# Kernel optimization log

Measured on AMD Instinct MI355X. Metric: run time of the kernel, lower is better.

Reference implementation:

```python
import jax, jax.numpy as jnp
import numpy as np

EMBED = 1024
HEADS = 16
HEAD_DIM = EMBED // HEADS
BATCH = 2
SEQ = 256

def setup_inputs() -> dict:
    key = jax.random.key(0)
    ks = jax.random.split(key, 6)
    x = jax.random.normal(ks[0], (BATCH, SEQ, EMBED), dtype=jnp.float32)
    s = 1.0 / np.sqrt(HEAD_DIM)
    Wq = jax.random.uniform(ks[1], (HEAD_DIM, HEAD_DIM), jnp.float32, -s, s)
    Wk = jax.random.uniform(ks[2], (HEAD_DIM, HEAD_DIM), jnp.float32, -s, s)
    Wv = jax.random.uniform(ks[3], (HEAD_DIM, HEAD_DIM), jnp.float32, -s, s)
    so = 1.0 / np.sqrt(EMBED)
    Wo = jax.random.uniform(ks[4], (EMBED, EMBED), jnp.float32, -so, so)
    bo = jax.random.uniform(ks[5], (EMBED,), jnp.float32, -so, so)
    return {"x": x, "Wq": Wq, "Wk": Wk, "Wv": Wv, "Wo": Wo, "bo": bo}

def reference(x, Wq, Wk, Wv, Wo, bo):
    n, s, e = x.shape
    xr = x.reshape(n, s, HEADS, HEAD_DIM)          # (n,s,h,d)
    # nn.Linear applies x @ W.T
    q = jnp.einsum('nshd,ed->nshe', xr, Wq)
    k = jnp.einsum('nshd,ed->nshe', xr, Wk)
    v = jnp.einsum('nshd,ed->nshe', xr, Wv)
    # elementwise outer-product score: (n,s,t,h,d), no reduction over d
    energy = q[:, :, None, :, :] * k[:, None, :, :, :]
    # NOTE: original code softmaxes over dim=3 == the HEADS axis
    attn = jax.nn.softmax(energy / jnp.float32(np.sqrt(EMBED)), axis=3)
    out = jnp.einsum('nsthd,nthd->nshd', attn, v)  # reduce over t
    out = out.reshape(n, s, HEADS * HEAD_DIM)
    return out @ Wo.T + bo
```

## Files before the change

kernel.cpp:

```cpp
#include <hip/hip_runtime.h>

#define NB 2
#define SQL 256
#define NH 16
#define HD 64
#define EMB 1024

typedef unsigned short ushortT;
typedef unsigned int uintT;
typedef __attribute__((ext_vector_type(8))) short bf16x8;
typedef __attribute__((ext_vector_type(4))) float f32x4;
typedef __attribute__((ext_vector_type(2))) float f32x2;

__device__ __constant__ float kQSCALE = 1.4426950408889634f / 32.0f;

__device__ __forceinline__ float fexp2(float x) { return __builtin_amdgcn_exp2f(x); }
__device__ __forceinline__ float frcp(float x)  { return __builtin_amdgcn_rcpf(x); }

__device__ __forceinline__ ushortT f2bf(float x) {
    uintT u = __float_as_uint(x);
    u += 0x7fffu + ((u >> 16) & 1u);
    return (ushortT)(u >> 16);
}
__device__ __forceinline__ ushort4 f2bf4(float4 a) {
    return make_ushort4(f2bf(a.x), f2bf(a.y), f2bf(a.z), f2bf(a.w));
}
__device__ __forceinline__ f32x2 unpk2(uintT u) {
    f32x2 r;
    r.x = __uint_as_float(u << 16);
    r.y = __uint_as_float(u & 0xffff0000u);
    return r;
}
__device__ __forceinline__ float pairsum_dpp(float u) {
    const int j = __builtin_amdgcn_mov_dpp(__float_as_int(u), 0xB1, 0xF, 0xF, true);
    return u + __int_as_float(j);
}

__global__ __launch_bounds__(256) void qkv_kernel(
    const float* __restrict__ x,
    const float* __restrict__ Wq,
    const float* __restrict__ Wk,
    const float* __restrict__ Wv,
    const float* __restrict__ Wo,
    const float* __restrict__ bo,
    ushortT* __restrict__ Q,
    ushortT* __restrict__ K,
    ushortT* __restrict__ V,
    float* __restrict__ AO,
    float* __restrict__ out,
    ushortT* __restrict__ Wob)
{
    __shared__ ushortT wls[3][64 * 72];
    __shared__ ushortT xs[2][16 * 72];

    const int tid = threadIdx.x;
    const int ns0 = blockIdx.x * 2;
    const int g   = blockIdx.x * 256 + tid;

    {
        const float4 z = make_float4(0.f, 0.f, 0.f, 0.f);
        ((float4*)AO)[g] = z;
        ((float4*)AO)[g + 65536] = z;
        const float4 bb = ((const float4*)bo)[g & 255];
        ((float4*)out)[g] = bb;
        ((float4*)out)[g + 65536] = bb;
    }
#pragma unroll
    for (int j = 0; j < 4; ++j) {
        const int f4 = j * 65536 + g;
        ((ushort4*)Wob)[f4] = f2bf4(((const float4*)Wo)[f4]);
    }

#pragma unroll
    for (int m = 0; m < 3; ++m) {
        const float4* src = (m == 0) ? (const float4*)Wq
                          : (m == 1) ? (const float4*)Wk : (const float4*)Wv;
#pragma unroll
        for (int j = 0; j < 4; ++j) {
            const int idx = j * 256 + tid;
            const int e   = idx >> 4;
            const int d4  = idx & 15;
            float4 a = src[idx];
            if (m == 0) { a.x *= kQSCALE; a.y *= kQSCALE; a.z *= kQSCALE; a.w *= kQSCALE; }
            *(ushort4*)&wls[m][e * 72 + d4 * 4] = f2bf4(a);
        }
    }
#pragma unroll
    for (int j = 0; j < 2; ++j) {
        const int idx = j * 256 + tid;
        const int r   = idx >> 8;
        const int h   = (idx >> 4) & 15;
        const int d4  = idx & 15;
        const float4 a = ((const float4*)(x + (size_t)(ns0 + r) * EMB))[idx & 255];
        *(ushort4*)&xs[r][h * 72 + d4 * 4] = f2bf4(a);
    }
    __syncthreads();

    const int w   = tid >> 6;
    const int nsr = w >> 1;
    const int eb0 = (w & 1) * 32;
    const int l   = tid & 63;
    const int lr  = l & 15;
    const int lk  = l >> 4;

    const bf16x8 a0 = *(const bf16x8*)&xs[nsr][lr * 72 + lk * 8];
    const bf16x8 a1 = *(const bf16x8*)&xs[nsr][lr * 72 + 32 + lk * 8];

#pragma unroll
    for (int m = 0; m < 3; ++m) {
        ushortT* outp = (m == 0) ? Q : (m == 1) ? K : V;
#pragma unroll
        for (int ef = 0; ef < 2; ++ef) {
            const int eb = eb0 + ef * 16;
            const bf16x8 b0 = *(const bf16x8*)&wls[m][(eb + lr) * 72 + lk * 8];
            const bf16x8 b1 = *(const bf16x8*)&wls[m][(eb + lr) * 72 + 32 + lk * 8];
            f32x4 c = {0.f, 0.f, 0.f, 0.f};
            c = __builtin_amdgcn_mfma_f32_16x16x32_bf16(a0, b0, c, 0, 0, 0);
            c = __builtin_amdgcn_mfma_f32_16x16x32_bf16(a1, b1, c, 0, 0, 0);
            ushortT* dst = outp + (size_t)(ns0 + nsr) * EMB + (eb + lr) * 16 + lk * 4;
            *(ushort4*)dst = make_ushort4(f2bf(c[0]), f2bf(c[1]), f2bf(c[2]), f2bf(c[3]));
        }
    }
}

#define ATTN_STEP(KU4, VU4)                                                    \
    {                                                                          \
        f32x2 k2[4], v2[4], p0[4], p1[4];                                      \
        k2[0] = unpk2(KU4.x); k2[1] = unpk2(KU4.y);                            \
        k2[2] = unpk2(KU4.z); k2[3] = unpk2(KU4.w);                            \
        _Pragma("unroll")                                                      \
        for (int j = 0; j < 4; ++j) {                                          \
            const f32x2 x0 = q0_2[j] * k2[j];                                  \
            const f32x2 x1 = q1_2[j] * k2[j];                                  \
            p0[j].x = fexp2(x0.x); p0[j].y = fexp2(x0.y);                      \
            p1[j].x = fexp2(x1.x); p1[j].y = fexp2(x1.y);                      \
        }                                                                      \
        const f32x2 s0 = (p0[0] + p0[1]) + (p0[2] + p0[3]);                    \
        const f32x2 s1 = (p1[0] + p1[1]) + (p1[2] + p1[3]);                    \
        const float rs0 = frcp(pairsum_dpp(s0.x + s0.y));                      \
        const float rs1 = frcp(pairsum_dpp(s1.x + s1.y));                      \
        const f32x2 rb0 = {rs0, rs0};                                          \
        const f32x2 rb1 = {rs1, rs1};                                          \
        v2[0] = unpk2(VU4.x); v2[1] = unpk2(VU4.y);                            \
        v2[2] = unpk2(VU4.z); v2[3] = unpk2(VU4.w);                            \
        _Pragma("unroll")                                                      \
        for (int j = 0; j < 4; ++j) {                                          \
            acc0[j] = __builtin_elementwise_fma(v2[j] * rb0, p0[j], acc0[j]);  \
            acc1[j] = __builtin_elementwise_fma(v2[j] * rb1, p1[j], acc1[j]);  \
        }                                                                      \
    }

__global__ __launch_bounds__(256) void attn_kernel(
    const ushortT* __restrict__ Q,
    const ushortT* __restrict__ K,
    const ushortT* __restrict__ V,
    float* __restrict__ AO)
{
    const int b    = blockIdx.x;
    const int tc   = b & 15;
    const int eh   = (b >> 4) & 1;
    const int st   = (b >> 5) & 31;
    const int n    = b >> 10;
    const int wave = threadIdx.x >> 6;
    const int l    = threadIdx.x & 63;
    const int s0   = st * 8 + wave * 2;
    const int t0   = tc * 16;

    f32x2 q0_2[4], q1_2[4];
    {
        const uint4* qp = (const uint4*)(Q + (size_t)(n * SQL + s0) * EMB + 512 * eh) + l;
        const uint4 qa = qp[0];
        const uint4 qb = qp[128];
        q0_2[0] = unpk2(qa.x); q0_2[1] = unpk2(qa.y);
        q0_2[2] = unpk2(qa.z); q0_2[3] = unpk2(qa.w);
        q1_2[0] = unpk2(qb.x); q1_2[1] = unpk2(qb.y);
        q1_2[2] = unpk2(qb.z); q1_2[3] = unpk2(qb.w);
    }

    f32x2 acc0[4], acc1[4];
#pragma unroll
    for (int j = 0; j < 4; ++j) {
        acc0[j] = (f32x2){0.f, 0.f};
        acc1[j] = (f32x2){0.f, 0.f};
    }

    const uint4* kp = (const uint4*)(K + (size_t)(n * SQL + t0) * EMB + 512 * eh) + l;
    const uint4* vp = (const uint4*)(V + (size_t)(n * SQL + t0) * EMB + 512 * eh) + l;

    uint4 ka = kp[0];
    uint4 kb = kp[128];
    uint4 va = vp[0];

#pragma unroll
    for (int tt = 0; tt < 16; tt += 2) {
        const uint4 kn2 = kp[256];
        const uint4 vb  = vp[128];
        ATTN_STEP(ka, va);
        const uint4 kn3 = kp[384];
        va = vp[256];
        kp += 256; vp += 256;
        ATTN_STEP(kb, vb);
        ka = kn2; kb = kn3;
    }

    float* base0 = AO + (size_t)(n * SQL + s0) * EMB + 512 * (l & 1) + 32 * eh + (l >> 1);
    float* base1 = base0 + EMB;
#pragma unroll
    for (int j = 0; j < 4; ++j) {
        atomicAdd(base0 + 64 * (2 * j),     acc0[j].x);
        atomicAdd(base0 + 64 * (2 * j + 1), acc0[j].y);
        atomicAdd(base1 + 64 * (2 * j),     acc1[j].x);
        atomicAdd(base1 + 64 * (2 * j + 1), acc1[j].y);
    }
}

__global__ __launch_bounds__(512) void proj_kernel(
    const float* __restrict__ AO,
    const ushortT* __restrict__ Wob,
    float* __restrict__ out)
{
    __shared__ ushortT As[64 * 40];
    __shared__ ushortT Bs[128 * 40];

    const int b  = blockIdx.x;
    const int kc = b & 3;
    const int jt = (b >> 2) & 7;
    const int rt = b >> 5;
    const int tid = threadIdx.x;
    const int r0 = rt * 64, j0 = jt * 128, k0 = kc * 256;

    const int w  = tid >> 6;
    const int wr = w >> 2;
    const int wc = w & 3;
    const int l  = tid & 63;
    const int lr = l & 15;
    const int lk = l >> 4;

    f32x4 c00 = {0.f, 0.f, 0.f, 0.f};
    f32x4 c01 = {0.f, 0.f, 0.f, 0.f};
    f32x4 c10 = {0.f, 0.f, 0.f, 0.f};
    f32x4 c11 = {0.f, 0.f, 0.f, 0.f};

    for (int kt = 0; kt < 8; ++kt) {
        const int kb = k0 + kt * 32;
        __syncthreads();
        {
            const int row = tid >> 3;
            const int kq  = tid & 7;
            const float4 a = *(const float4*)&AO[(size_t)(r0 + row) * EMB + kb + kq * 4];
            *(ushort4*)&As[row * 40 + kq * 4] = f2bf4(a);
        }
        {
            const int row = tid >> 2;
            const int ko  = tid & 3;
            const uint4 wv = *(const uint4*)&Wob[(size_t)(j0 + row) * EMB + kb + ko * 8];
            *(uint4*)&Bs[row * 40 + ko * 8] = wv;
        }
        __syncthreads();

        const bf16x8 a0 = *(const bf16x8*)&As[(wr * 32 + lr) * 40 + lk * 8];
        const bf16x8 a1 = *(const bf16x8*)&As[(wr * 32 + 16 + lr) * 40 + lk * 8];
        const bf16x8 b0 = *(const bf16x8*)&Bs[(wc * 32 + lr) * 40 + lk * 8];
        const bf16x8 b1 = *(const bf16x8*)&Bs[(wc * 32 + 16 + lr) * 40 + lk * 8];
        c00 = __builtin_amdgcn_mfma_f32_16x16x32_bf16(a0, b0, c00, 0, 0, 0);
        c01 = __builtin_amdgcn_mfma_f32_16x16x32_bf16(a0, b1, c01, 0, 0, 0);
        c10 = __builtin_amdgcn_mfma_f32_16x16x32_bf16(a1, b0, c10, 0, 0, 0);
        c11 = __builtin_amdgcn_mfma_f32_16x16x32_bf16(a1, b1, c11, 0, 0, 0);
    }

    const int rbase = r0 + wr * 32 + lk * 4;
    const int jbase = j0 + wc * 32 + lr;
#pragma unroll
    for (int e = 0; e < 4; ++e) {
        atomicAdd(&out[(size_t)(rbase + e) * EMB + jbase],           c00[e]);
        atomicAdd(&out[(size_t)(rbase + e) * EMB + jbase + 16],      c01[e]);
        atomicAdd(&out[(size_t)(rbase + 16 + e) * EMB + jbase],      c10[e]);
        atomicAdd(&out[(size_t)(rbase + 16 + e) * EMB + jbase + 16], c11[e]);
    }
}

extern "C" void kernel_launch(void* const* d_in, const int* in_sizes, int n_in,
                              void* d_out, int out_size, void* d_ws, size_t ws_size,
                              hipStream_t stream)
{
    const float* x  = (const float*)d_in[0];
    const float* Wq = (const float*)d_in[1];
    const float* Wk = (const float*)d_in[2];
    const float* Wv = (const float*)d_in[3];
    const float* Wo = (const float*)d_in[4];
    const float* bo = (const float*)d_in[5];

    float* ws = (float*)d_ws;
    ushortT* Q   = (ushortT*)ws;
    ushortT* K   = (ushortT*)(ws + 262144);
    ushortT* V   = (ushortT*)(ws + 524288);
    float*   AO  = ws + 786432;
    ushortT* Wob = (ushortT*)(ws + 1310720);

    qkv_kernel<<<256, 256, 0, stream>>>(x, Wq, Wk, Wv, Wo, bo, Q, K, V, AO,
                                        (float*)d_out, Wob);
    attn_kernel<<<2048, 256, 0, stream>>>(Q, K, V, AO);
    proj_kernel<<<256, 512, 0, stream>>>(AO, Wob, (float*)d_out);
}
```

Before: 58.76 us.

## Split attention over t across waves and reduce in LDS before atomics

Each block now handles two query rows per (batch, head-half) with its four waves covering different 32-key slices of a 128-key half, instead of each wave taking its own query rows over 16 keys. Partial accumulators are summed through shared memory and written with a quarter as many global atomics. The grid is halved and each wave runs twice as many loop iterations. This adds a barrier and 16 KB of LDS per block.

```diff
diff --git a/kernel.cpp b/kernel.cpp
--- a/kernel.cpp
+++ b/kernel.cpp
@@ -135,10 +135,10 @@
             p0[j].x = fexp2(x0.x); p0[j].y = fexp2(x0.y);                      \
             p1[j].x = fexp2(x1.x); p1[j].y = fexp2(x1.y);                      \
         }                                                                      \
-        const f32x2 s0 = (p0[0] + p0[1]) + (p0[2] + p0[3]);                    \
-        const f32x2 s1 = (p1[0] + p1[1]) + (p1[2] + p1[3]);                    \
-        const float rs0 = frcp(pairsum_dpp(s0.x + s0.y));                      \
-        const float rs1 = frcp(pairsum_dpp(s1.x + s1.y));                      \
+        const f32x2 s0v = (p0[0] + p0[1]) + (p0[2] + p0[3]);                   \
+        const f32x2 s1v = (p1[0] + p1[1]) + (p1[2] + p1[3]);                   \
+        const float rs0 = frcp(pairsum_dpp(s0v.x + s0v.y));                    \
+        const float rs1 = frcp(pairsum_dpp(s1v.x + s1v.y));                    \
         const f32x2 rb0 = {rs0, rs0};                                          \
         const f32x2 rb1 = {rs1, rs1};                                          \
         v2[0] = unpk2(VU4.x); v2[1] = unpk2(VU4.y);                            \
@@ -156,15 +156,17 @@
     const ushortT* __restrict__ V,
     float* __restrict__ AO)
 {
+    __shared__ float red[16][256];
+
     const int b    = blockIdx.x;
-    const int tc   = b & 15;
-    const int eh   = (b >> 4) & 1;
-    const int st   = (b >> 5) & 31;
-    const int n    = b >> 10;
+    const int tw   = b & 1;
+    const int eh   = (b >> 1) & 1;
+    const int sg   = (b >> 2) & 127;
+    const int n    = b >> 9;
     const int wave = threadIdx.x >> 6;
     const int l    = threadIdx.x & 63;
-    const int s0   = st * 8 + wave * 2;
-    const int t0   = tc * 16;
+    const int s0   = sg * 2;
+    const int t0   = tw * 128 + wave * 32;
 
     f32x2 q0_2[4], q1_2[4];
     {
@@ -192,7 +194,7 @@
     uint4 va = vp[0];
 
 #pragma unroll
-    for (int tt = 0; tt < 16; tt += 2) {
+    for (int tt = 0; tt < 32; tt += 2) {
         const uint4 kn2 = kp[256];
         const uint4 vb  = vp[128];
         ATTN_STEP(ka, va);
@@ -203,14 +205,23 @@
         ka = kn2; kb = kn3;
     }
 
-    float* base0 = AO + (size_t)(n * SQL + s0) * EMB + 512 * (l & 1) + 32 * eh + (l >> 1);
-    float* base1 = base0 + EMB;
 #pragma unroll
     for (int j = 0; j < 4; ++j) {
-        atomicAdd(base0 + 64 * (2 * j),     acc0[j].x);
-        atomicAdd(base0 + 64 * (2 * j + 1), acc0[j].y);
-        atomicAdd(base1 + 64 * (2 * j),     acc1[j].x);
-        atomicAdd(base1 + 64 * (2 * j + 1), acc1[j].y);
+        red[2 * j    ][wave * 64 + l] = acc0[j].x;
+        red[2 * j + 1][wave * 64 + l] = acc0[j].y;
+        red[8 + 2 * j    ][wave * 64 + l] = acc1[j].x;
+        red[8 + 2 * j + 1][wave * 64 + l] = acc1[j].y;
+    }
+    __syncthreads();
+
+    float* aob = AO + (size_t)(n * SQL + s0) * EMB + 512 * (l & 1) + 32 * eh + (l >> 1);
+#pragma unroll
+    for (int di = 0; di < 4; ++di) {
+        const int i = wave * 4 + di;
+        const float sum = (red[i][l] + red[i][64 + l]) + (red[i][128 + l] + red[i][192 + l]);
+        const int s = i >> 3;
+        const int c = i & 7;
+        atomicAdd(aob + (size_t)s * EMB + 64 * c, sum);
     }
 }
 
@@ -299,6 +310,6 @@
 
     qkv_kernel<<<256, 256, 0, stream>>>(x, Wq, Wk, Wv, Wo, bo, Q, K, V, AO,
                                         (float*)d_out, Wob);
-    attn_kernel<<<2048, 256, 0, stream>>>(Q, K, V, AO);
+    attn_kernel<<<1024, 256, 0, stream>>>(Q, K, V, AO);
     proj_kernel<<<256, 512, 0, stream>>>(AO, Wob, (float*)d_out);
 }
```

After: 50.04 us. 14.9% less time.
